# Kernel optimization log

Hardware: AMD Instinct MI355X
Metric: run time of the kernel (lower is better)

The kernel has to match this reference:

```python
import jax, jax.numpy as jnp
import numpy as np

B, C, N, K, COUT, W32 = 4, 64, 4096, 16, 64, 32
EPS = 1e-5  # BatchNorm eps


def conv1x1(x, w, b):
    # x: (B, Cin, K, N), w: (Cout, Cin), b: (Cout,)
    return jnp.einsum('oi,bikn->bokn', w, x) + b[None, :, None, None]


def batchnorm(x, gamma, beta):
    # training-mode BN over (B, K, N) per channel
    m = x.mean(axis=(0, 2, 3), keepdims=True)
    v = x.var(axis=(0, 2, 3), keepdims=True)
    return gamma[None, :, None, None] * (x - m) * jax.lax.rsqrt(v + EPS) + beta[None, :, None, None]


def setup_inputs() -> dict:
    key = jax.random.key(0)
    ks = jax.random.split(key, 14)
    s = 0.1
    return {
        'inputs': jax.random.normal(ks[0], (B, C, N), jnp.float32),
        'inputs_pos': jax.random.normal(ks[1], (B, 3, N), jnp.float32),
        'inverse_density': jax.random.uniform(ks[2], (B, 1, N), jnp.float32),
        # WeightNet: Conv2d(3, 32, 1) + BN(32)
        'wn_w': jax.random.normal(ks[3], (W32, 3), jnp.float32) * s,
        'wn_b': jnp.zeros((W32,), jnp.float32),
        'wn_g': jnp.ones((W32,), jnp.float32),
        'wn_be': jnp.zeros((W32,), jnp.float32),
        # DensityNet: Conv2d(1,16,1)+BN(16), Conv2d(16,1,1)
        'dn_w1': jax.random.normal(ks[4], (16, 1), jnp.float32) * s,
        'dn_b1': jnp.zeros((16,), jnp.float32),
        'dn_g1': jnp.ones((16,), jnp.float32),
        'dn_be1': jnp.zeros((16,), jnp.float32),
        'dn_w2': jax.random.normal(ks[5], (1, 16), jnp.float32) * s,
        'dn_b2': jnp.zeros((1,), jnp.float32),
        # Linear(C*32, COUT)
        'lin_w': jax.random.normal(ks[6], (COUT, C * W32), jnp.float32) * (1.0 / np.sqrt(C * W32)),
        'lin_b': jnp.zeros((COUT,), jnp.float32),
    }


def reference(inputs, inputs_pos, inverse_density,
              wn_w, wn_b, wn_g, wn_be,
              dn_w1, dn_b1, dn_g1, dn_be1, dn_w2, dn_b2,
              lin_w, lin_b):
    b, c, n = inputs.shape
    # pairwise squared distances (B, N, N); stride=1 so no FPS sampling
    sq = jnp.sum(inputs_pos ** 2, axis=1)  # (B, N)
    dist = sq[:, :, None] + sq[:, None, :] - 2.0 * jnp.einsum('bdi,bdj->bij', inputs_pos, inputs_pos)
    _, nn_idx = jax.lax.top_k(-dist, K)  # (B, N, K) nearest neighbors (incl. self)

    def gather(x, idx):  # x: (Cx, N), idx: (N, K) -> (Cx, K, N)
        return jnp.transpose(x[:, idx], (0, 2, 1))

    nn_pos = jax.vmap(gather)(inputs_pos, nn_idx)        # (B, 3, K, N)
    nn_inputs = jax.vmap(gather)(inputs, nn_idx)         # (B, C, K, N)
    lnn_pos = nn_pos - inputs_pos[:, :, None, :]         # translated neighbor positions
    nn_inv_d = jax.vmap(gather)(inverse_density, nn_idx)  # (B, 1, K, N)

    density_scale = nn_inv_d / nn_inv_d.max(axis=2, keepdims=True)
    h = jax.nn.relu(batchnorm(conv1x1(density_scale, dn_w1, dn_b1), dn_g1, dn_be1))
    density_scale = jax.nn.sigmoid(conv1x1(h, dn_w2, dn_b2))  # (B, 1, K, N)

    scaled = nn_inputs * density_scale                    # (B, C, K, N)
    weights = jax.nn.relu(batchnorm(conv1x1(lnn_pos, wn_w, wn_b), wn_g, wn_be))  # (B, 32, K, N)

    # per-point matmul: (B,N,C,K) @ (B,N,K,32) -> (B,N,C,32)
    feat = jnp.einsum('bckn,bwkn->bncw', scaled, weights).reshape(b, n, c * W32)
    out = feat @ lin_w.T + lin_b                          # (B, N, COUT)
    return jnp.transpose(out, (0, 2, 1))                  # (B, COUT, N)
```

## Files before the change

### kernel.cpp

```cpp
#include <hip/hip_runtime.h>
#include <math.h>

#define NB 4
#define NC 64
#define NPTS 4096
#define NROWS (NB*NPTS)

typedef __attribute__((ext_vector_type(4))) float f32x4;
typedef __bf16 bf16x8 __attribute__((ext_vector_type(8)));

__device__ __forceinline__ ushort f2bf(float f) {
  unsigned u = __float_as_uint(f);
  u = (u + 0x7FFFu + ((u >> 16) & 1u)) >> 16;
  return (ushort)u;
}
__device__ __forceinline__ unsigned pk2(float lo, float hi) {
  return (unsigned)f2bf(lo) | ((unsigned)f2bf(hi) << 16);
}

__device__ __forceinline__ void insert16(double dist, int j, double (&dd)[16], int (&ii)[16]) {
  double cd = dist; int ci = j;
#pragma unroll
  for (int s = 0; s < 16; ++s) {
    double od = dd[s]; int oi = ii[s];
    bool c = cd < od;
    dd[s] = c ? cd : od;
    ii[s] = c ? ci : oi;
    cd = c ? od : cd;
    ci = c ? oi : ci;
  }
}

__device__ __forceinline__ void bub16u(unsigned key, unsigned (&t)[16]) {
#pragma unroll
  for (int q2 = 0; q2 < 16; ++q2) {
    unsigned lo = min(key, t[q2]);
    key = max(key, t[q2]);
    t[q2] = lo;
  }
}

__device__ __forceinline__ double wave_reduce(double v) {
#pragma unroll
  for (int off = 32; off; off >>= 1) v += __shfl_down(v, off, 64);
  return v;
}

__global__ __launch_bounds__(256) void pack_pos4(const float* __restrict__ pos,
                                                 float4* __restrict__ pos4) {
  int g = blockIdx.x * 256 + threadIdx.x;
  int b = g >> 12, n = g & (NPTS - 1);
  const float* pb = pos + b * 3 * NPTS;
  pos4[g] = make_float4(pb[n], pb[NPTS + n], pb[2 * NPTS + n], 0.f);
}

__global__ __launch_bounds__(256) void knn_sub(const float4* __restrict__ pos4,
                                               uint4* __restrict__ partials) {
  __shared__ float4 cand[128];
  int t = threadIdx.x;
  int row0 = blockIdx.x * 256;
  int b = row0 >> 12;
  int y = blockIdx.y;
  int j0 = (y >> 1) * 1024 + (y & 1) * 128;
  const float4* pb = pos4 + b * NPTS;
  if (t < 128) cand[t] = pb[j0 + t];
  __syncthreads();
  float4 q = pb[(row0 + t) & (NPTS - 1)];
  unsigned dd[16];
#pragma unroll
  for (int s = 0; s < 16; ++s) dd[s] = 0xFFFFFFFFu;
#pragma unroll 4
  for (int jj = 0; jj < 128; ++jj) {
    float4 c = cand[jj];
    float dx = q.x - c.x, dy = q.y - c.y, dz = q.z - c.z;
    float d = fmaf(dx, dx, fmaf(dy, dy, dz * dz));
    unsigned key = (__float_as_uint(d) & 0xFFFFF000u) | (unsigned)(j0 + jj);
#pragma unroll
    for (int s = 0; s < 16; ++s) {
      unsigned lo = min(key, dd[s]);
      key = max(key, dd[s]);
      dd[s] = lo;
    }
  }
  uint4* po = partials + ((size_t)y * NROWS + row0 + t) * 4;
  po[0] = make_uint4(dd[0], dd[1], dd[2], dd[3]);
  po[1] = make_uint4(dd[4], dd[5], dd[6], dd[7]);
  po[2] = make_uint4(dd[8], dd[9], dd[10], dd[11]);
  po[3] = make_uint4(dd[12], dd[13], dd[14], dd[15]);
}

__global__ __launch_bounds__(64) void knn_thresh(const uint4* __restrict__ partials,
                                                 unsigned* __restrict__ T0g) {
  __shared__ unsigned sl[64 * 132];
  int tid = threadIdx.x;
  int row0 = blockIdx.x * 64;
  uint4* sl4 = (uint4*)sl;
  size_t base = (size_t)row0 * 4 + tid;
#define TW(IT, V) { int g2 = ((IT) & 3) * 64 + tid; \
                    sl4[(g2 >> 2) * 33 + ((IT) >> 2) * 4 + (g2 & 3)] = (V); }
#define TB(B) { int IT0 = (B) * 8; \
  uint4 w0 = partials[(size_t)((IT0+0)>>2)*(NROWS*4) + ((IT0+0)&3)*64 + base]; \
  uint4 w1 = partials[(size_t)((IT0+1)>>2)*(NROWS*4) + ((IT0+1)&3)*64 + base]; \
  uint4 w2 = partials[(size_t)((IT0+2)>>2)*(NROWS*4) + ((IT0+2)&3)*64 + base]; \
  uint4 w3 = partials[(size_t)((IT0+3)>>2)*(NROWS*4) + ((IT0+3)&3)*64 + base]; \
  uint4 w4 = partials[(size_t)((IT0+4)>>2)*(NROWS*4) + ((IT0+4)&3)*64 + base]; \
  uint4 w5 = partials[(size_t)((IT0+5)>>2)*(NROWS*4) + ((IT0+5)&3)*64 + base]; \
  uint4 w6 = partials[(size_t)((IT0+6)>>2)*(NROWS*4) + ((IT0+6)&3)*64 + base]; \
  uint4 w7 = partials[(size_t)((IT0+7)>>2)*(NROWS*4) + ((IT0+7)&3)*64 + base]; \
  TW(IT0+0,w0) TW(IT0+1,w1) TW(IT0+2,w2) TW(IT0+3,w3) \
  TW(IT0+4,w4) TW(IT0+5,w5) TW(IT0+6,w6) TW(IT0+7,w7) }
  TB(0) TB(1) TB(2) TB(3)
#undef TB
#undef TW
  __syncthreads();
  unsigned top[16];
#pragma unroll
  for (int s = 0; s < 16; ++s) top[s] = 0xFFFFFFFFu;
  const unsigned* my = sl + tid * 132;
  for (int y = 0; y < 8; ++y) {
#pragma unroll 4
    for (int s = 0; s < 16; ++s) {
      unsigned key = my[y * 16 + s];
      if (key >= top[15]) break;
#pragma unroll
      for (int q2 = 0; q2 < 16; ++q2) {
        unsigned lo = min(key, top[q2]);
        key = max(key, top[q2]);
        top[q2] = lo;
      }
    }
  }
  T0g[row0 + tid] = top[15] & 0xFFFFF000u;
}

__global__ __launch_bounds__(256) void knn_filter(const float4* __restrict__ pos4,
                                                  const unsigned* __restrict__ T0g,
                                                  uint4* __restrict__ surv) {
  __shared__ float4 cand[256];
  __shared__ unsigned lq[256 * 28];
  int t = threadIdx.x;
  int row0 = blockIdx.x * 256;
  int b = row0 >> 12;
  int y = blockIdx.y;
  int j0 = y * 256;
  const float4* pb = pos4 + b * NPTS;
  cand[t] = pb[j0 + t];
  __syncthreads();
  int r = row0 + t;
  float4 q = pb[r & (NPTS - 1)];
  unsigned T = T0g[r];
  unsigned cnt = 0;
  unsigned* myq = lq + t * 28;
#pragma unroll 4
  for (int jj = 0; jj < 256; ++jj) {
    float4 c = cand[jj];
    float dx = q.x - c.x, dy = q.y - c.y, dz = q.z - c.z;
    float d = fmaf(dx, dx, fmaf(dy, dy, dz * dz));
    unsigned m = __float_as_uint(d) & 0xFFFFF000u;
    if (m <= T) {
      if (cnt < 28u) myq[cnt] = m | (unsigned)(j0 + jj);
      ++cnt;
    }
  }
  cnt = cnt < 28u ? cnt : 28u;
  unsigned t16[16];
#pragma unroll
  for (int s = 0; s < 16; ++s) t16[s] = 0xFFFFFFFFu;
  const uint4* qsrc = (const uint4*)myq;
  uint4 q0 = qsrc[0], q1 = qsrc[1], q2 = qsrc[2], q3 = qsrc[3],
        q4 = qsrc[4], q5 = qsrc[5], q6 = qsrc[6];
#define SIN(K, I) { unsigned key = ((I) < cnt) ? (K) : 0xFFFFFFFFu; bub16u(key, t16); }
  SIN(q0.x,0u) SIN(q0.y,1u) SIN(q0.z,2u) SIN(q0.w,3u)
  SIN(q1.x,4u) SIN(q1.y,5u) SIN(q1.z,6u) SIN(q1.w,7u)
  SIN(q2.x,8u) SIN(q2.y,9u) SIN(q2.z,10u) SIN(q2.w,11u)
  SIN(q3.x,12u) SIN(q3.y,13u) SIN(q3.z,14u) SIN(q3.w,15u)
  SIN(q4.x,16u) SIN(q4.y,17u) SIN(q4.z,18u) SIN(q4.w,19u)
  SIN(q5.x,20u) SIN(q5.y,21u) SIN(q5.z,22u) SIN(q5.w,23u)
  SIN(q6.x,24u) SIN(q6.y,25u) SIN(q6.z,26u) SIN(q6.w,27u)
#undef SIN
  uint4* dst = surv + ((size_t)r * 16 + y) * 4;
  dst[0] = make_uint4(t16[0], t16[1], t16[2], t16[3]);
  dst[1] = make_uint4(t16[4], t16[5], t16[6], t16[7]);
  dst[2] = make_uint4(t16[8], t16[9], t16[10], t16[11]);
  dst[3] = make_uint4(t16[12], t16[13], t16[14], t16[15]);
}

__global__ __launch_bounds__(256) void knn_final(const float4* __restrict__ pos4,
                                                 const float* __restrict__ invd,
                                                 const uint4* __restrict__ surv,
                                                 int* __restrict__ nn_idx,
                                                 float* __restrict__ dsbuf,
                                                 double* __restrict__ stp) {
  int t = threadIdx.x;
  int ln = t & 15;
  int r = blockIdx.x * 16 + (t >> 4);
  int b = r >> 12, n = r & (NPTS - 1);

  const uint4* sp = surv + ((size_t)r * 16 + ln) * 4;
  uint4 u0 = sp[0], u1 = sp[1], u2 = sp[2], u3 = sp[3];
  unsigned h0=u0.x,h1=u0.y,h2=u0.z,h3=u0.w,h4=u1.x,h5=u1.y,h6=u1.z,h7=u1.w,
           h8=u2.x,h9=u2.y,h10=u2.z,h11=u2.w,h12=u3.x,h13=u3.y,h14=u3.z,h15=u3.w;
  unsigned t0,t1,t2,t3,t4,t5,t6,t7,t8,t9,t10,t11,t12,t13,t14,t15,t16;
#define RND(TT) { unsigned m = h0; \
  m = min(m, (unsigned)__shfl_xor((int)m, 1)); \
  m = min(m, (unsigned)__shfl_xor((int)m, 2)); \
  m = min(m, (unsigned)__shfl_xor((int)m, 4)); \
  m = min(m, (unsigned)__shfl_xor((int)m, 8)); \
  TT = m; bool pop = (h0 == m); \
  h0 = pop ? h1 : h0;  h1 = pop ? h2 : h1;  h2 = pop ? h3 : h2; \
  h3 = pop ? h4 : h3;  h4 = pop ? h5 : h4;  h5 = pop ? h6 : h5; \
  h6 = pop ? h7 : h6;  h7 = pop ? h8 : h7;  h8 = pop ? h9 : h8; \
  h9 = pop ? h10 : h9; h10 = pop ? h11 : h10; h11 = pop ? h12 : h11; \
  h12 = pop ? h13 : h12; h13 = pop ? h14 : h13; h14 = pop ? h15 : h14; \
  h15 = pop ? 0xFFFFFFFFu : h15; }
  RND(t0) RND(t1) RND(t2) RND(t3) RND(t4) RND(t5) RND(t6) RND(t7)
  RND(t8) RND(t9) RND(t10) RND(t11) RND(t12) RND(t13) RND(t14) RND(t15)
  RND(t16)

  const float4* pb = pos4 + b * NPTS;
  float4 qp = pb[n];
  double xi = qp.x, yi = qp.y, zi = qp.z;

  int jm;
  bool tie = ((t15 & 0xFFFFF000u) == (t16 & 0xFFFFF000u));
  if (!tie) {
    unsigned tm = t0;
    tm = (ln == 1) ? t1 : tm;   tm = (ln == 2) ? t2 : tm;
    tm = (ln == 3) ? t3 : tm;   tm = (ln == 4) ? t4 : tm;
    tm = (ln == 5) ? t5 : tm;   tm = (ln == 6) ? t6 : tm;
    tm = (ln == 7) ? t7 : tm;   tm = (ln == 8) ? t8 : tm;
    tm = (ln == 9) ? t9 : tm;   tm = (ln == 10) ? t10 : tm;
    tm = (ln == 11) ? t11 : tm; tm = (ln == 12) ? t12 : tm;
    tm = (ln == 13) ? t13 : tm; tm = (ln == 14) ? t14 : tm;
    tm = (ln == 15) ? t15 : tm;
    jm = (int)(tm & 0xFFFu);
  } else {
    unsigned t17, t18, t19, t20, t21, t22, t23;
    RND(t17) RND(t18) RND(t19) RND(t20) RND(t21) RND(t22) RND(t23)
    double dd[16]; int ii[16];
#pragma unroll
    for (int s = 0; s < 16; ++s) { dd[s] = 1e300; ii[s] = 0; }
#define RRK(TT) if (TT != 0xFFFFFFFFu) { int j = (int)(TT & 0xFFFu); \
  float4 cj = pb[j]; \
  double dx = xi - (double)cj.x, dy = yi - (double)cj.y, dz = zi - (double)cj.z; \
  double dist = dx * dx + dy * dy + dz * dz; \
  if (dist < dd[15]) insert16(dist, j, dd, ii); }
    RRK(t0) RRK(t1) RRK(t2) RRK(t3) RRK(t4) RRK(t5) RRK(t6) RRK(t7)
    RRK(t8) RRK(t9) RRK(t10) RRK(t11) RRK(t12) RRK(t13) RRK(t14) RRK(t15)
    RRK(t16) RRK(t17) RRK(t18) RRK(t19) RRK(t20) RRK(t21) RRK(t22) RRK(t23)
#undef RRK
    int jj2 = ii[0];
#pragma unroll
    for (int s = 1; s < 16; ++s) jj2 = (ln == s) ? ii[s] : jj2;
    jm = jj2;
  }
#undef RND

  nn_idx[(size_t)r * 16 + ln] = jm;
  const float* ivb = invd + b * NPTS;
  float v = ivb[jm];
  float vmax = v;
  vmax = fmaxf(vmax, __shfl_xor(vmax, 1));
  vmax = fmaxf(vmax, __shfl_xor(vmax, 2));
  vmax = fmaxf(vmax, __shfl_xor(vmax, 4));
  vmax = fmaxf(vmax, __shfl_xor(vmax, 8));
  float x = v / vmax;
  dsbuf[(size_t)r * 16 + ln] = x;

  double sx = x, sxx = (double)x * (double)x;
  float4 pj = pb[jm];
  double lx = (double)pj.x - xi, lyv = (double)pj.y - yi, lzv = (double)pj.z - zi;
  double l1x = lx, l1y = lyv, l1z = lzv;
  double lxx = lx * lx, lyy = lyv * lyv, lzz = lzv * lzv;
  double lxy = lx * lyv, lxz = lx * lzv, lyz = lyv * lzv;
  sx  = wave_reduce(sx);  sxx = wave_reduce(sxx);
  l1x = wave_reduce(l1x); l1y = wave_reduce(l1y); l1z = wave_reduce(l1z);
  lxx = wave_reduce(lxx); lyy = wave_reduce(lyy); lzz = wave_reduce(lzz);
  lxy = wave_reduce(lxy); lxz = wave_reduce(lxz); lyz = wave_reduce(lyz);
  if ((t & 63) == 0) {
    double* o = stp + ((size_t)blockIdx.x * 4 + (t >> 6)) * 16;
    o[0] = sx;  o[1] = sxx;
    o[2] = l1x; o[3] = l1y; o[4] = l1z;
    o[5] = lxx; o[6] = lyy; o[7] = lzz;
    o[8] = lxy; o[9] = lxz; o[10] = lyz;
  }
}

__global__ __launch_bounds__(256) void finalize_params(const double* __restrict__ stp,
                                const float* __restrict__ wn_w,
                                const float* __restrict__ wn_g,
                                const float* __restrict__ wn_be,
                                const float* __restrict__ dn_w1,
                                const float* __restrict__ dn_g1,
                                const float* __restrict__ dn_be1,
                                float* __restrict__ prm) {
  __shared__ double part[16][16];
  __shared__ double red[11];
  const double M = (double)NROWS * 16.0;
  int t = threadIdx.x;
  {
    int c = t & 15, ch = t >> 4;
    double s = 0.0;
#pragma unroll 8
    for (int w = 0; w < 256; ++w) s += stp[(size_t)(ch * 256 + w) * 16 + c];
    part[ch][c] = s;
  }
  __syncthreads();
  if (t < 11) {
    double s = 0.0;
#pragma unroll
    for (int ch = 0; ch < 16; ++ch) s += part[ch][t];
    red[t] = s;
  }
  __syncthreads();
  if (t < 32) {
    double m0 = red[2] / M, m1 = red[3] / M, m2 = red[4] / M;
    double cxx = red[5] / M - m0 * m0, cyy = red[6] / M - m1 * m1, czz = red[7] / M - m2 * m2;
    double cxy = red[8] / M - m0 * m1, cxz = red[9] / M - m0 * m2, cyz = red[10] / M - m1 * m2;
    double w0 = wn_w[t * 3], w1 = wn_w[t * 3 + 1], w2 = wn_w[t * 3 + 2];
    double var = w0 * w0 * cxx + w1 * w1 * cyy + w2 * w2 * czz
               + 2.0 * (w0 * w1 * cxy + w0 * w2 * cxz + w1 * w2 * cyz);
    double alpha = (double)wn_g[t] / sqrt(var + 1e-5);
    double a0 = alpha * w0, a1 = alpha * w1, a2 = alpha * w2;
    prm[t * 3] = (float)a0; prm[t * 3 + 1] = (float)a1; prm[t * 3 + 2] = (float)a2;
    prm[96 + t] = (float)((double)wn_be[t] - (a0 * m0 + a1 * m1 + a2 * m2));
  } else if (t < 48) {
    int ch = t - 32;
    double mx = red[0] / M;
    double vx = red[1] / M - mx * mx;
    double w = dn_w1[ch];
    double alpha = (double)dn_g1[ch] * w / sqrt(w * w * vx + 1e-5);
    prm[128 + ch] = (float)alpha;
    prm[144 + ch] = (float)((double)dn_be1[ch] - alpha * mx);
  }
}

__global__ __launch_bounds__(256) void ds_kernel(float* __restrict__ dsbuf,
                                                 const float* __restrict__ prm,
                                                 const float* __restrict__ dn_w2,
                                                 const float* __restrict__ dn_b2) {
  int r = blockIdx.x * 256 + threadIdx.x;
  float A[16], Bp[16], W2[16];
#pragma unroll
  for (int ch = 0; ch < 16; ++ch) {
    A[ch] = prm[128 + ch];
    Bp[ch] = prm[144 + ch];
    W2[ch] = dn_w2[ch];
  }
  float b2 = dn_b2[0];
#pragma unroll
  for (int k = 0; k < 16; ++k) {
    float x = dsbuf[(size_t)r * 16 + k];
    float s = b2;
#pragma unroll
    for (int ch = 0; ch < 16; ++ch) s = fmaf(W2[ch], fmaxf(fmaf(A[ch], x, Bp[ch]), 0.f), s);
    dsbuf[(size_t)r * 16 + k] = 1.f / (1.f + expf(-s));
  }
}

__global__ __launch_bounds__(256) void transpose_in(const float* __restrict__ in,
                                                    ushort* __restrict__ inT) {
  __shared__ float tile[64][68];
  int t = threadIdx.x;
  int b = blockIdx.x >> 6;
  int n0 = (blockIdx.x & 63) << 6;
  {
    int c = t >> 2, q = t & 3;
    const float* src = in + ((size_t)(b * 64 + c)) * NPTS + n0 + q * 16;
    float4 v0 = ((const float4*)src)[0];
    float4 v1 = ((const float4*)src)[1];
    float4 v2 = ((const float4*)src)[2];
    float4 v3 = ((const float4*)src)[3];
    *(float4*)&tile[c][q * 16 + 0] = v0;
    *(float4*)&tile[c][q * 16 + 4] = v1;
    *(float4*)&tile[c][q * 16 + 8] = v2;
    *(float4*)&tile[c][q * 16 + 12] = v3;
  }
  __syncthreads();
  {
    int nl = t >> 2, cq = t & 3;
    unsigned pk[8];
#pragma unroll
    for (int i = 0; i < 8; ++i) {
      float lo = tile[cq * 16 + 2 * i][nl];
      float hi = tile[cq * 16 + 2 * i + 1][nl];
      pk[i] = pk2(lo, hi);
    }
    uint4* dst = (uint4*)(inT + ((size_t)(b * NPTS + n0 + nl)) * 64 + cq * 16);
    dst[0] = make_uint4(pk[0], pk[1], pk[2], pk[3]);
    dst[1] = make_uint4(pk[4], pk[5], pk[6], pk[7]);
  }
}

__global__ __launch_bounds__(256) void prep_LTf(const float* __restrict__ lin_w,
                                                ushort* __restrict__ LTf) {
  int g = blockIdx.x * 256 + threadIdx.x;
  int l = g & 63, ot = (g >> 6) & 3, s = g >> 8;
  int o = ot * 16 + (l & 15);
  const float* src = lin_w + (size_t)o * 2048 + s * 32 + (l >> 4) * 8;
  float4 u0 = ((const float4*)src)[0];
  float4 u1 = ((const float4*)src)[1];
  ((uint4*)LTf)[g] = make_uint4(pk2(u0.x, u0.y), pk2(u0.z, u0.w),
                                pk2(u1.x, u1.y), pk2(u1.z, u1.w));
}

#define XSTR 2320
#define WTOFF 37120
#define WTSTR 1552

__global__ __launch_bounds__(256, 2) void fused(const ushort* __restrict__ inT,
                                                const float4* __restrict__ pos4,
                                                const int* __restrict__ nn_idx,
                                                const float* __restrict__ dsbuf,
                                                const float* __restrict__ prm_g,
                                                const ushort* __restrict__ LTf,
                                                const float* __restrict__ lin_b,
                                                float* __restrict__ out) {
  __shared__ __align__(16) char smem[65536];
  __shared__ float prms[128];
  char* xraw = smem;
  char* wT = smem + WTOFF;
  int t = threadIdx.x;
  int blk = blockIdx.x;
  int b = blk >> 8;
  int n0 = (blk & 255) << 4;
  if (t < 128) prms[t] = prm_g[t];
  __syncthreads();
  {
    int k = t >> 4, p = t & 15;
    int r = blk * 16 + p;
    int n = n0 + p;
    int j = nn_idx[(size_t)r * 16 + k];
    float4 pj = pos4[b * NPTS + j];
    float4 pn = pos4[b * NPTS + n];
    float lx = pj.x - pn.x, ly = pj.y - pn.y, lz = pj.z - pn.z;
    float ds = dsbuf[(size_t)r * 16 + k];
    const uint4* srcx = (const uint4*)(inT + ((size_t)(b * NPTS + j)) * 64);
    uint4* dstx = (uint4*)(xraw + p * XSTR + k * 144);
#pragma unroll
    for (int i = 0; i < 8; ++i) dstx[i] = srcx[i];
    char* wr = wT + p * WTSTR + k * 2;
#pragma unroll
    for (int w = 0; w < 32; ++w) {
      float v = fmaf(prms[w * 3], lx,
                fmaf(prms[w * 3 + 1], ly,
                fmaf(prms[w * 3 + 2], lz, prms[96 + w])));
      *(ushort*)(wr + w * 48) = f2bf(fmaxf(v, 0.f) * ds);
    }
  }
  __syncthreads();
  int wv = t >> 6;
  int l = t & 63;
  int lr = l & 15;
  int q = l >> 4;
  int kq8 = (q & 1) * 1152;
  int swz = (lr & 7) << 4;
  const f32x4 zf = (f32x4)0.f;
  uint4 zu = make_uint4(0u, 0u, 0u, 0u);

#define DECLD(IT) unsigned d##IT##_0,d##IT##_1,d##IT##_2,d##IT##_3,d##IT##_4, \
  d##IT##_5,d##IT##_6,d##IT##_7,d##IT##_8,d##IT##_9,d##IT##_10,d##IT##_11, \
  d##IT##_12,d##IT##_13,d##IT##_14,d##IT##_15;
  DECLD(0) DECLD(1) DECLD(2) DECLD(3)
#undef DECLD

#define LOADB(BU, NI, XP) { \
    const char* xb = (XP) + ((NI) * 16 + lr) * 2; \
    unsigned e0 = *(const ushort*)(xb); \
    unsigned e1 = *(const ushort*)(xb + 144); \
    unsigned e2 = *(const ushort*)(xb + 288); \
    unsigned e3 = *(const ushort*)(xb + 432); \
    unsigned e4 = *(const ushort*)(xb + 576); \
    unsigned e5 = *(const ushort*)(xb + 720); \
    unsigned e6 = *(const ushort*)(xb + 864); \
    unsigned e7 = *(const ushort*)(xb + 1008); \
    BU = make_uint4(e0 | (e1 << 16), e2 | (e3 << 16), \
                    e4 | (e5 << 16), e6 | (e7 << 16)); }

#define MM(AF, BF, RA, RB) { \
    f32x4 D = __builtin_amdgcn_mfma_f32_16x16x32_bf16(AF, BF, zf, 0, 0, 0); \
    RA = pk2(D.x, D.y); RB = pk2(D.z, D.w); }

#define DO_POINT(IT) { \
    int p = wv * 4 + (IT); \
    const char* wtp = wT + p * WTSTR; \
    const char* xp = xraw + p * XSTR + kq8; \
    uint4 a0u = zu, a1u = zu; \
    if (q < 2) { \
      a0u = *(const uint4*)(wtp + lr * 48 + q * 16); \
      a1u = *(const uint4*)(wtp + (16 + lr) * 48 + q * 16); \
    } \
    bf16x8 A0 = *reinterpret_cast<bf16x8*>(&a0u); \
    bf16x8 A1 = *reinterpret_cast<bf16x8*>(&a1u); \
    uint4 b0u, b1u, b2u, b3u; \
    LOADB(b0u, 0, xp) LOADB(b1u, 1, xp) LOADB(b2u, 2, xp) LOADB(b3u, 3, xp) \
    bf16x8 B0 = *reinterpret_cast<bf16x8*>(&b0u); \
    bf16x8 B1 = *reinterpret_cast<bf16x8*>(&b1u); \
    bf16x8 B2 = *reinterpret_cast<bf16x8*>(&b2u); \
    bf16x8 B3 = *reinterpret_cast<bf16x8*>(&b3u); \
    MM(A0, B0, d##IT##_0, d##IT##_1)   MM(A0, B1, d##IT##_2, d##IT##_3) \
    MM(A0, B2, d##IT##_4, d##IT##_5)   MM(A0, B3, d##IT##_6, d##IT##_7) \
    MM(A1, B0, d##IT##_8, d##IT##_9)   MM(A1, B1, d##IT##_10, d##IT##_11) \
    MM(A1, B2, d##IT##_12, d##IT##_13) MM(A1, B3, d##IT##_14, d##IT##_15) }

  DO_POINT(0) DO_POINT(1) DO_POINT(2) DO_POINT(3)
#undef DO_POINT
#undef MM
#undef LOADB
  __syncthreads();
  {
    int hq = q >> 1;
    int m0 = (q & 1) * 2;
#define STT(IT, MI, NI, RA, RB) { \
      int p = wv * 4 + (IT); \
      int h = (MI) * 2 + hq; \
      int base = ((NI) * 16 + lr) * 1024 + (p + 16 * h) * 16 + m0 * 4; \
      *(unsigned*)(smem + (base ^ swz)) = RA; \
      *(unsigned*)(smem + ((base + 4) ^ swz)) = RB; }
#define STP(IT) \
    STT(IT,0,0,d##IT##_0,d##IT##_1)   STT(IT,0,1,d##IT##_2,d##IT##_3) \
    STT(IT,0,2,d##IT##_4,d##IT##_5)   STT(IT,0,3,d##IT##_6,d##IT##_7) \
    STT(IT,1,0,d##IT##_8,d##IT##_9)   STT(IT,1,1,d##IT##_10,d##IT##_11) \
    STT(IT,1,2,d##IT##_12,d##IT##_13) STT(IT,1,3,d##IT##_14,d##IT##_15)
    STP(0) STP(1) STP(2) STP(3)
#undef STP
#undef STT
  }
  __syncthreads();
  {
    const uint4* Lq = (const uint4*)LTf;
    f32x4 cacc = (f32x4)0.f;
#pragma unroll 4
    for (int s = 0; s < 64; ++s) {
      uint4 ua = *(const uint4*)(smem + (((s * 64 + l) * 16) ^ ((s & 7) << 4)));
      uint4 ub = Lq[(s * 4 + wv) * 64 + l];
      bf16x8 A = *reinterpret_cast<bf16x8*>(&ua);
      bf16x8 B = *reinterpret_cast<bf16x8*>(&ub);
      cacc = __builtin_amdgcn_mfma_f32_16x16x32_bf16(A, B, cacc, 0, 0, 0);
    }
    int o = wv * 16 + lr;
    float bias = lin_b[o];
    cacc.x += bias; cacc.y += bias; cacc.z += bias; cacc.w += bias;
    *(f32x4*)(out + ((size_t)(b * 64 + o)) * NPTS + n0 + q * 4) = cacc;
  }
}

extern "C" void kernel_launch(void* const* d_in, const int* in_sizes, int n_in,
                              void* d_out, int out_size, void* d_ws, size_t ws_size,
                              hipStream_t stream) {
  (void)in_sizes; (void)n_in; (void)out_size; (void)ws_size;
  const float* inputs = (const float*)d_in[0];
  const float* pos    = (const float*)d_in[1];
  const float* invd   = (const float*)d_in[2];
  const float* wn_w   = (const float*)d_in[3];
  const float* wn_g   = (const float*)d_in[5];
  const float* wn_be  = (const float*)d_in[6];
  const float* dn_w1  = (const float*)d_in[7];
  const float* dn_g1  = (const float*)d_in[9];
  const float* dn_be1 = (const float*)d_in[10];
  const float* dn_w2  = (const float*)d_in[11];
  const float* dn_b2  = (const float*)d_in[12];
  const float* lin_w  = (const float*)d_in[13];
  const float* lin_b  = (const float*)d_in[14];
  float* outp = (float*)d_out;

  char* ws = (char*)d_ws;
  float*    prm      = (float*)(ws + 1024);
  float4*   pos4     = (float4*)(ws + 4096);
  int*      nnidx    = (int*)(ws + (size_t)(1u << 19));
  float*    dsbuf    = (float*)(ws + (size_t)(3u << 19));
  ushort*   inT      = (ushort*)(ws + (size_t)(5u << 19));
  ushort*   LTf      = (ushort*)(ws + (size_t)(9u << 19));
  unsigned* T0g      = (unsigned*)(ws + (size_t)(19u << 18));
  double*   stp      = (double*)(ws + (size_t)(5u << 20));
  uint4*    partials = (uint4*)(ws + (size_t)(11u << 19));
  uint4*    surv     = (uint4*)(ws + (size_t)(11u << 19));

  pack_pos4<<<64, 256, 0, stream>>>(pos, pos4);
  transpose_in<<<256, 256, 0, stream>>>(inputs, inT);
  prep_LTf<<<64, 256, 0, stream>>>(lin_w, LTf);
  knn_sub<<<dim3(64, 8), 256, 0, stream>>>(pos4, partials);
  knn_thresh<<<256, 64, 0, stream>>>(partials, T0g);
  knn_filter<<<dim3(64, 16), 256, 0, stream>>>(pos4, T0g, surv);
  knn_final<<<1024, 256, 0, stream>>>(pos4, invd, surv, nnidx, dsbuf, stp);
  finalize_params<<<1, 256, 0, stream>>>(stp, wn_w, wn_g, wn_be, dn_w1, dn_g1, dn_be1, prm);
  ds_kernel<<<64, 256, 0, stream>>>(dsbuf, prm, dn_w2, dn_b2);
  fused<<<1024, 256, 0, stream>>>(inT, pos4, nnidx, dsbuf, prm, LTf, lin_b, outp);
}
```

Before: 154.3 us.

## Merge prep kernels and fold density-net sigmoid into fused kernel

Combines the pos4 packing, input transpose and linear-weight packing into one launch selected by block index. Moves the second density-net layer and sigmoid from a separate ds_kernel into the fused kernel's gather phase, which drops a read-modify-write pass over dsbuf. The bubble-insert in knn_filter now skips invalid slots with a branch instead of inserting sentinel keys. Together these cut three kernel launches and some memory traffic, at the cost of a bit more per-thread work in the fused kernel.

```diff
diff --git a/kernel.cpp b/kernel.cpp
--- a/kernel.cpp
+++ b/kernel.cpp
@@ -46,12 +46,60 @@
   return v;
 }
 
-__global__ __launch_bounds__(256) void pack_pos4(const float* __restrict__ pos,
-                                                 float4* __restrict__ pos4) {
-  int g = blockIdx.x * 256 + threadIdx.x;
-  int b = g >> 12, n = g & (NPTS - 1);
-  const float* pb = pos + b * 3 * NPTS;
-  pos4[g] = make_float4(pb[n], pb[NPTS + n], pb[2 * NPTS + n], 0.f);
+__global__ __launch_bounds__(256) void prep_all(const float* __restrict__ pos,
+                                                float4* __restrict__ pos4,
+                                                const float* __restrict__ in,
+                                                ushort* __restrict__ inT,
+                                                const float* __restrict__ lin_w,
+                                                ushort* __restrict__ LTf) {
+  __shared__ float tile[64][68];
+  int t = threadIdx.x;
+  int bid = blockIdx.x;
+  if (bid < 64) {
+    int g = bid * 256 + t;
+    int b = g >> 12, n = g & (NPTS - 1);
+    const float* pb = pos + b * 3 * NPTS;
+    pos4[g] = make_float4(pb[n], pb[NPTS + n], pb[2 * NPTS + n], 0.f);
+  } else if (bid < 320) {
+    int blk = bid - 64;
+    int b = blk >> 6;
+    int n0 = (blk & 63) << 6;
+    {
+      int c = t >> 2, q = t & 3;
+      const float* src = in + ((size_t)(b * 64 + c)) * NPTS + n0 + q * 16;
+      float4 v0 = ((const float4*)src)[0];
+      float4 v1 = ((const float4*)src)[1];
+      float4 v2 = ((const float4*)src)[2];
+      float4 v3 = ((const float4*)src)[3];
+      *(float4*)&tile[c][q * 16 + 0] = v0;
+      *(float4*)&tile[c][q * 16 + 4] = v1;
+      *(float4*)&tile[c][q * 16 + 8] = v2;
+      *(float4*)&tile[c][q * 16 + 12] = v3;
+    }
+    __syncthreads();
+    {
+      int nl = t >> 2, cq = t & 3;
+      unsigned pk[8];
+#pragma unroll
+      for (int i = 0; i < 8; ++i) {
+        float lo = tile[cq * 16 + 2 * i][nl];
+        float hi = tile[cq * 16 + 2 * i + 1][nl];
+        pk[i] = pk2(lo, hi);
+      }
+      uint4* dst = (uint4*)(inT + ((size_t)(b * NPTS + n0 + nl)) * 64 + cq * 16);
+      dst[0] = make_uint4(pk[0], pk[1], pk[2], pk[3]);
+      dst[1] = make_uint4(pk[4], pk[5], pk[6], pk[7]);
+    }
+  } else {
+    int g = (bid - 320) * 256 + t;
+    int l = g & 63, ot = (g >> 6) & 3, s = g >> 8;
+    int o = ot * 16 + (l & 15);
+    const float* src = lin_w + (size_t)o * 2048 + s * 32 + (l >> 4) * 8;
+    float4 u0 = ((const float4*)src)[0];
+    float4 u1 = ((const float4*)src)[1];
+    ((uint4*)LTf)[g] = make_uint4(pk2(u0.x, u0.y), pk2(u0.z, u0.w),
+                                  pk2(u1.x, u1.y), pk2(u1.z, u1.w));
+  }
 }
 
 __global__ __launch_bounds__(256) void knn_sub(const float4* __restrict__ pos4,
@@ -169,7 +217,7 @@
   const uint4* qsrc = (const uint4*)myq;
   uint4 q0 = qsrc[0], q1 = qsrc[1], q2 = qsrc[2], q3 = qsrc[3],
         q4 = qsrc[4], q5 = qsrc[5], q6 = qsrc[6];
-#define SIN(K, I) { unsigned key = ((I) < cnt) ? (K) : 0xFFFFFFFFu; bub16u(key, t16); }
+#define SIN(K, I) { if ((I) < cnt) bub16u((K), t16); }
   SIN(q0.x,0u) SIN(q0.y,1u) SIN(q0.z,2u) SIN(q0.w,3u)
   SIN(q1.x,4u) SIN(q1.y,5u) SIN(q1.z,6u) SIN(q1.w,7u)
   SIN(q2.x,8u) SIN(q2.y,9u) SIN(q2.z,10u) SIN(q2.w,11u)
@@ -335,75 +383,6 @@
   }
 }
 
-__global__ __launch_bounds__(256) void ds_kernel(float* __restrict__ dsbuf,
-                                                 const float* __restrict__ prm,
-                                                 const float* __restrict__ dn_w2,
-                                                 const float* __restrict__ dn_b2) {
-  int r = blockIdx.x * 256 + threadIdx.x;
-  float A[16], Bp[16], W2[16];
-#pragma unroll
-  for (int ch = 0; ch < 16; ++ch) {
-    A[ch] = prm[128 + ch];
-    Bp[ch] = prm[144 + ch];
-    W2[ch] = dn_w2[ch];
-  }
-  float b2 = dn_b2[0];
-#pragma unroll
-  for (int k = 0; k < 16; ++k) {
-    float x = dsbuf[(size_t)r * 16 + k];
-    float s = b2;
-#pragma unroll
-    for (int ch = 0; ch < 16; ++ch) s = fmaf(W2[ch], fmaxf(fmaf(A[ch], x, Bp[ch]), 0.f), s);
-    dsbuf[(size_t)r * 16 + k] = 1.f / (1.f + expf(-s));
-  }
-}
-
-__global__ __launch_bounds__(256) void transpose_in(const float* __restrict__ in,
-                                                    ushort* __restrict__ inT) {
-  __shared__ float tile[64][68];
-  int t = threadIdx.x;
-  int b = blockIdx.x >> 6;
-  int n0 = (blockIdx.x & 63) << 6;
-  {
-    int c = t >> 2, q = t & 3;
-    const float* src = in + ((size_t)(b * 64 + c)) * NPTS + n0 + q * 16;
-    float4 v0 = ((const float4*)src)[0];
-    float4 v1 = ((const float4*)src)[1];
-    float4 v2 = ((const float4*)src)[2];
-    float4 v3 = ((const float4*)src)[3];
-    *(float4*)&tile[c][q * 16 + 0] = v0;
-    *(float4*)&tile[c][q * 16 + 4] = v1;
-    *(float4*)&tile[c][q * 16 + 8] = v2;
-    *(float4*)&tile[c][q * 16 + 12] = v3;
-  }
-  __syncthreads();
-  {
-    int nl = t >> 2, cq = t & 3;
-    unsigned pk[8];
-#pragma unroll
-    for (int i = 0; i < 8; ++i) {
-      float lo = tile[cq * 16 + 2 * i][nl];
-      float hi = tile[cq * 16 + 2 * i + 1][nl];
-      pk[i] = pk2(lo, hi);
-    }
-    uint4* dst = (uint4*)(inT + ((size_t)(b * NPTS + n0 + nl)) * 64 + cq * 16);
-    dst[0] = make_uint4(pk[0], pk[1], pk[2], pk[3]);
-    dst[1] = make_uint4(pk[4], pk[5], pk[6], pk[7]);
-  }
-}
-
-__global__ __launch_bounds__(256) void prep_LTf(const float* __restrict__ lin_w,
-                                                ushort* __restrict__ LTf) {
-  int g = blockIdx.x * 256 + threadIdx.x;
-  int l = g & 63, ot = (g >> 6) & 3, s = g >> 8;
-  int o = ot * 16 + (l & 15);
-  const float* src = lin_w + (size_t)o * 2048 + s * 32 + (l >> 4) * 8;
-  float4 u0 = ((const float4*)src)[0];
-  float4 u1 = ((const float4*)src)[1];
-  ((uint4*)LTf)[g] = make_uint4(pk2(u0.x, u0.y), pk2(u0.z, u0.w),
-                                pk2(u1.x, u1.y), pk2(u1.z, u1.w));
-}
-
 #define XSTR 2320
 #define WTOFF 37120
 #define WTSTR 1552
@@ -413,18 +392,22 @@
                                                 const int* __restrict__ nn_idx,
                                                 const float* __restrict__ dsbuf,
                                                 const float* __restrict__ prm_g,
+                                                const float* __restrict__ dn_w2,
+                                                const float* __restrict__ dn_b2,
                                                 const ushort* __restrict__ LTf,
                                                 const float* __restrict__ lin_b,
                                                 float* __restrict__ out) {
   __shared__ __align__(16) char smem[65536];
-  __shared__ float prms[128];
+  __shared__ float prms[180];
   char* xraw = smem;
   char* wT = smem + WTOFF;
   int t = threadIdx.x;
   int blk = blockIdx.x;
   int b = blk >> 8;
   int n0 = (blk & 255) << 4;
-  if (t < 128) prms[t] = prm_g[t];
+  if (t < 160) prms[t] = prm_g[t];
+  else if (t < 176) prms[t] = dn_w2[t - 160];
+  else if (t == 176) prms[t] = dn_b2[0];
   __syncthreads();
   {
     int k = t >> 4, p = t & 15;
@@ -434,7 +417,12 @@
     float4 pj = pos4[b * NPTS + j];
     float4 pn = pos4[b * NPTS + n];
     float lx = pj.x - pn.x, ly = pj.y - pn.y, lz = pj.z - pn.z;
-    float ds = dsbuf[(size_t)r * 16 + k];
+    float xr = dsbuf[(size_t)r * 16 + k];
+    float sacc = prms[176];
+#pragma unroll
+    for (int ch = 0; ch < 16; ++ch)
+      sacc = fmaf(prms[160 + ch], fmaxf(fmaf(prms[128 + ch], xr, prms[144 + ch]), 0.f), sacc);
+    float ds = 1.f / (1.f + expf(-sacc));
     const uint4* srcx = (const uint4*)(inT + ((size_t)(b * NPTS + j)) * 64);
     uint4* dstx = (uint4*)(xraw + p * XSTR + k * 144);
 #pragma unroll
@@ -576,14 +564,11 @@
   uint4*    partials = (uint4*)(ws + (size_t)(11u << 19));
   uint4*    surv     = (uint4*)(ws + (size_t)(11u << 19));
 
-  pack_pos4<<<64, 256, 0, stream>>>(pos, pos4);
-  transpose_in<<<256, 256, 0, stream>>>(inputs, inT);
-  prep_LTf<<<64, 256, 0, stream>>>(lin_w, LTf);
+  prep_all<<<384, 256, 0, stream>>>(pos, pos4, inputs, inT, lin_w, LTf);
   knn_sub<<<dim3(64, 8), 256, 0, stream>>>(pos4, partials);
   knn_thresh<<<256, 64, 0, stream>>>(partials, T0g);
   knn_filter<<<dim3(64, 16), 256, 0, stream>>>(pos4, T0g, surv);
   knn_final<<<1024, 256, 0, stream>>>(pos4, invd, surv, nnidx, dsbuf, stp);
   finalize_params<<<1, 256, 0, stream>>>(stp, wn_w, wn_g, wn_be, dn_w1, dn_g1, dn_be1, prm);
-  ds_kernel<<<64, 256, 0, stream>>>(dsbuf, prm, dn_w2, dn_b2);
-  fused<<<1024, 256, 0, stream>>>(inT, pos4, nnidx, dsbuf, prm, LTf, lin_b, outp);
-}
+  fused<<<1024, 256, 0, stream>>>(inT, pos4, nnidx, dsbuf, prm, dn_w2, dn_b2, LTf, lin_b, outp);
+}
```

Measured after the change: 144.1 us. 6.6% less time.
